# Kernel optimization log

Measured on AMD Instinct MI355X. Metric: run time of the kernel, lower is better.

## Reference

```python
import jax, jax.numpy as jnp
import numpy as np

L, D = 2048, 1024
D_INNER = 2 * D          # expand=2
D_STATE = 16
D_CONV = 4
DT_RANK = D // 16        # ceil(1024/16) = 64
HID = 4 * D
EPS = 1e-5


def _layernorm(x, g, b):
    mu = jnp.mean(x, axis=-1, keepdims=True)
    var = jnp.mean(jnp.square(x - mu), axis=-1, keepdims=True)
    return (x - mu) * jax.lax.rsqrt(var + EPS) * g + b


def setup_inputs() -> dict:
    key = jax.random.key(0)
    ks = jax.random.split(key, 12)
    f = lambda k, sh, s=0.02: (jax.random.normal(k, sh, jnp.float32) * s)
    return {
        "x": jax.random.normal(ks[0], (L, D), jnp.float32),
        "ln1_g": jnp.ones((D,), jnp.float32),
        "ln1_b": jnp.zeros((D,), jnp.float32),
        "ln2_g": jnp.ones((D,), jnp.float32),
        "ln2_b": jnp.zeros((D,), jnp.float32),
        "in_proj_w": f(ks[1], (2 * D_INNER, D)),
        "conv_w": f(ks[2], (D_INNER, D_CONV), 0.1),
        "conv_b": jnp.zeros((D_INNER,), jnp.float32),
        "x_proj_w": f(ks[3], (DT_RANK + 2 * D_STATE, D_INNER)),
        "dt_proj_w": f(ks[4], (D_INNER, DT_RANK), 0.1),
        "dt_proj_b": f(ks[5], (D_INNER,), 0.1),
        "A_log": jnp.log(jnp.broadcast_to(
            jnp.arange(1, D_STATE + 1, dtype=jnp.float32), (D_INNER, D_STATE))),
        "D_param": jnp.ones((D_INNER,), jnp.float32),
        "out_proj_w": f(ks[6], (D, D_INNER)),
        "ffn_w1": f(ks[7], (HID, D)),
        "ffn_b1": jnp.zeros((HID,), jnp.float32),
        "ffn_w2": f(ks[8], (D, HID)),
        "ffn_b2": jnp.zeros((D,), jnp.float32),
    }


def _mamba(x, in_proj_w, conv_w, conv_b, x_proj_w, dt_proj_w, dt_proj_b,
           A_log, D_param, out_proj_w):
    # x: (L, D)
    xz = x @ in_proj_w.T                    # (L, 2*d_inner)
    xm, z = xz[:, :D_INNER], xz[:, D_INNER:]
    # causal depthwise conv1d, kernel d_conv, output length L
    xp = jnp.pad(xm, ((D_CONV - 1, 0), (0, 0)))
    xc = conv_b
    for k in range(D_CONV):                 # 4 taps, fixed small loop
        xc = xc + xp[k:k + L] * conv_w[None, :, k]
    xc = jax.nn.silu(xc)                    # (L, d_inner)
    proj = xc @ x_proj_w.T                  # (L, dt_rank + 2*d_state)
    dt = proj[:, :DT_RANK]
    B = proj[:, DT_RANK:DT_RANK + D_STATE]  # (L, d_state)
    C = proj[:, DT_RANK + D_STATE:]         # (L, d_state)
    delta = jax.nn.softplus(dt @ dt_proj_w.T + dt_proj_b)  # (L, d_inner)
    A = -jnp.exp(A_log)                     # (d_inner, d_state)
    dA = jnp.exp(delta[:, :, None] * A[None])               # (L, d_inner, d_state)
    dBx = delta[:, :, None] * B[:, None, :] * xc[:, :, None]

    def step(h, inp):
        dA_t, dBx_t, C_t = inp
        h = h * dA_t + dBx_t                # (d_inner, d_state)
        y = jnp.einsum('ds,s->d', h, C_t)
        return h, y

    h0 = jnp.zeros((D_INNER, D_STATE), x.dtype)
    _, ys = jax.lax.scan(step, h0, (dA, dBx, C))            # ys: (L, d_inner)
    y = ys + xc * D_param
    y = y * jax.nn.silu(z)
    return y @ out_proj_w.T                 # (L, D)


def reference(x, ln1_g, ln1_b, ln2_g, ln2_b, in_proj_w, conv_w, conv_b,
              x_proj_w, dt_proj_w, dt_proj_b, A_log, D_param, out_proj_w,
              ffn_w1, ffn_b1, ffn_w2, ffn_b2):
    residual = x
    h = _layernorm(x, ln1_g, ln1_b)
    h = _mamba(h, in_proj_w, conv_w, conv_b, x_proj_w, dt_proj_w, dt_proj_b,
               A_log, D_param, out_proj_w)
    h = h + residual
    # FFN has an internal residual around the normed input, plus outer residual
    n = _layernorm(h, ln2_g, ln2_b)
    f = n + (jax.nn.relu(n @ ffn_w1.T + ffn_b1) @ ffn_w2.T + ffn_b2)
    return h + f
```

## Files before the change

### kernel.cpp

```cpp
#include <hip/hip_runtime.h>
#include <hip/hip_bf16.h>
#include <math.h>

#define L_SEQ 2048
#define DMODEL 1024
#define DINNER 2048
#define DSTATE 16
#define DTRANK 64
#define NHID 4096
#define NC 64
#define LC 32

typedef __bf16 bf16_t;
typedef __bf16 bf16x4 __attribute__((ext_vector_type(4)));
typedef __bf16 bf16x8 __attribute__((ext_vector_type(8)));
typedef float f32x4 __attribute__((ext_vector_type(4)));

#define WAIT_VM0 0x0F70

__device__ __forceinline__ void async_cp16(const bf16_t* g, bf16_t* l) {
    __builtin_amdgcn_global_load_lds(
        (const __attribute__((address_space(1))) void*)g,
        (__attribute__((address_space(3))) void*)l, 16, 0, 0);
}

template <int EPI, int SPLIT>
__global__ __launch_bounds__(512, 4) void gemm_big(
    const bf16_t* __restrict__ A, int lda,
    const bf16_t* __restrict__ W, int ldw,
    bf16_t* __restrict__ C, int ldc,
    int Kslice, long cstride,
    const float* __restrict__ bias)
{
    __shared__ bf16_t As[2 * 8192];
    __shared__ bf16_t Ws[2 * 4096];

    const int tid  = threadIdx.x;
    const int lane = tid & 63;
    const int w    = tid >> 6;

    int my, mx, kz;
    if (SPLIT == 0) {
        int lid = blockIdx.y * 32 + blockIdx.x;
        int r = lid & 7, i = lid >> 3;
        my = (r >> 2) * 4 + (i & 3);
        mx = (r & 3) * 8 + (i >> 2);
        kz = 0;
    } else {
        int id = (blockIdx.z * 8 + blockIdx.y) * 8 + blockIdx.x;
        int r = id & 7, i = id >> 3;
        kz = r >> 1;
        my = i & 7;
        mx = (r & 1) * 4 + (i >> 3);
    }
    const int m0 = my * 256;
    const int n0 = mx * 128;
    const int k0 = kz * Kslice;

    const int p    = lane & 3;
    const int rA0  = 2 * w * 16 + (lane >> 2);
    const int rA1  = rA0 + 16;
    const int rW   = w * 16 + (lane >> 2);
    const int dcA0 = (p - ((rA0 >> 1) & 3)) & 3;
    const int dcA1 = (p - ((rA1 >> 1) & 3)) & 3;
    const int dcW  = (p - ((rW  >> 1) & 3)) & 3;

    const bf16_t* gA0 = A + (size_t)(m0 + rA0) * lda + k0 + dcA0 * 8;
    const bf16_t* gA1 = A + (size_t)(m0 + rA1) * lda + k0 + dcA1 * 8;
    const bf16_t* gW  = W + (size_t)(n0 + rW) * ldw + k0 + dcW * 8;
    const int aLo0 = (2 * w) * 512;
    const int aLo1 = aLo0 + 512;
    const int wLo  = w * 512;

    const int wr   = w >> 1;
    const int wc   = w & 1;
    const int quad = lane >> 4;
    const int lr   = lane & 15;
    int offA[4], offW[4];
    #pragma unroll
    for (int i = 0; i < 4; ++i) {
        int ra = wr * 64 + i * 16 + lr;
        offA[i] = ra * 32 + (((quad + ((ra >> 1) & 3)) & 3) * 8);
        int rb = wc * 64 + i * 16 + lr;
        offW[i] = rb * 32 + (((quad + ((rb >> 1) & 3)) & 3) * 8);
    }

    const int niter = Kslice >> 5;

    async_cp16(gA0, &As[aLo0]);
    async_cp16(gA1, &As[aLo1]);
    async_cp16(gW,  &Ws[wLo]);
    gA0 += 32; gA1 += 32; gW += 32;

    f32x4 acc[4][4] = {};
    for (int it = 0; it < niter; ++it) {
        __builtin_amdgcn_s_waitcnt(WAIT_VM0);
        __builtin_amdgcn_s_barrier();
        asm volatile("" ::: "memory");

        if (it + 1 < niter) {
            int sa = ((it + 1) & 1) * 8192;
            int sw = ((it + 1) & 1) * 4096;
            async_cp16(gA0, &As[sa + aLo0]);
            async_cp16(gA1, &As[sa + aLo1]);
            async_cp16(gW,  &Ws[sw + wLo]);
            gA0 += 32; gA1 += 32; gW += 32;
        }

        const int ca = (it & 1) * 8192;
        const int cw = (it & 1) * 4096;
        bf16x8 af[4], bw[4];
        #pragma unroll
        for (int i = 0; i < 4; ++i) af[i] = *(const bf16x8*)&As[ca + offA[i]];
        #pragma unroll
        for (int j = 0; j < 4; ++j) bw[j] = *(const bf16x8*)&Ws[cw + offW[j]];
        #pragma unroll
        for (int i = 0; i < 4; ++i)
            #pragma unroll
            for (int j = 0; j < 4; ++j)
                acc[i][j] = __builtin_amdgcn_mfma_f32_16x16x32_bf16(af[i], bw[j], acc[i][j], 0, 0, 0);
    }

    bf16_t* Cb = C + (size_t)kz * cstride;
    #pragma unroll
    for (int i = 0; i < 4; ++i) {
        int row0 = m0 + wr * 64 + i * 16 + quad * 4;
        #pragma unroll
        for (int j = 0; j < 4; ++j) {
            int col = n0 + wc * 64 + j * 16 + lr;
            float bv = (EPI == 2) ? bias[col] : 0.f;
            #pragma unroll
            for (int r = 0; r < 4; ++r) {
                float v = acc[i][j][r];
                if (EPI == 2) v = fmaxf(v + bv, 0.f);
                Cb[(size_t)(row0 + r) * ldc + col] = (bf16_t)v;
            }
        }
    }
}

template <int EPI, int OUTBF16>
__global__ __launch_bounds__(256) void gemm_simple(
    const bf16_t* __restrict__ A, int lda,
    const bf16_t* __restrict__ W, int ldw,
    void* __restrict__ Cv, int ldc,
    int N, int Kslice, long cstride,
    const float* __restrict__ bias)
{
    __shared__ bf16_t As[128 * 72];
    __shared__ bf16_t Ws[128 * 72];

    const int tid  = threadIdx.x;
    const int lane = tid & 63;
    const int w    = tid >> 6;
    const int m0   = blockIdx.y * 128;
    const int n0   = blockIdx.x * 128;
    const int kz   = blockIdx.z;
    const int k0   = kz * Kslice;

    const int wr   = w >> 1;
    const int wc   = w & 1;
    const int quad = lane >> 4;
    const int lr   = lane & 15;

    f32x4 acc[4][4] = {};

    for (int k = 0; k < Kslice; k += 64) {
        __syncthreads();
        #pragma unroll
        for (int i = 0; i < 4; ++i) {
            int idx = tid + i * 256;
            int row = idx >> 3;
            int c8  = (idx & 7) * 8;
            *(bf16x8*)&As[row * 72 + c8] =
                *(const bf16x8*)(A + (size_t)(m0 + row) * lda + k0 + k + c8);
            int gn = n0 + row; if (gn > N - 1) gn = N - 1;
            *(bf16x8*)&Ws[row * 72 + c8] =
                *(const bf16x8*)(W + (size_t)gn * ldw + k0 + k + c8);
        }
        __syncthreads();

        #pragma unroll
        for (int kk = 0; kk < 64; kk += 32) {
            bf16x8 af[4], bw[4];
            #pragma unroll
            for (int i = 0; i < 4; ++i)
                af[i] = *(const bf16x8*)&As[(wr * 64 + i * 16 + lr) * 72 + kk + quad * 8];
            #pragma unroll
            for (int j = 0; j < 4; ++j)
                bw[j] = *(const bf16x8*)&Ws[(wc * 64 + j * 16 + lr) * 72 + kk + quad * 8];
            #pragma unroll
            for (int i = 0; i < 4; ++i)
                #pragma unroll
                for (int j = 0; j < 4; ++j)
                    acc[i][j] = __builtin_amdgcn_mfma_f32_16x16x32_bf16(af[i], bw[j], acc[i][j], 0, 0, 0);
        }
    }

    float*  Cf = (float*)Cv + (size_t)kz * cstride;
    bf16_t* Cb = (bf16_t*)Cv + (size_t)kz * cstride;
    #pragma unroll
    for (int i = 0; i < 4; ++i) {
        int row0 = m0 + wr * 64 + i * 16 + quad * 4;
        #pragma unroll
        for (int j = 0; j < 4; ++j) {
            int col = n0 + wc * 64 + j * 16 + lr;
            if (col < N) {
                float bv = (EPI == 3) ? bias[col] : 0.f;
                #pragma unroll
                for (int r = 0; r < 4; ++r) {
                    float v = acc[i][j][r];
                    if (EPI == 3) {
                        float t = v + bv;
                        v = fmaxf(t, 0.f) + log1pf(__expf(-fabsf(t)));
                    }
                    size_t o = (size_t)(row0 + r) * ldc + col;
                    if (OUTBF16) Cb[o] = (bf16_t)v;
                    else         Cf[o] = v;
                }
            }
        }
    }
}

__global__ __launch_bounds__(256) void cvt_ln1(
    const float* __restrict__ s0, const float* __restrict__ s1,
    const float* __restrict__ s2, const float* __restrict__ s3,
    const float* __restrict__ s4, const float* __restrict__ s5,
    bf16_t* __restrict__ dst,
    const float* __restrict__ x, const float* __restrict__ g,
    const float* __restrict__ b, bf16_t* __restrict__ outb)
{
    if (blockIdx.x < 14656) {
        int e = (blockIdx.x * 256 + threadIdx.x) * 4;
        const float* src; int local;
        if      (e < 4194304)  { src = s0; local = e; }
        else if (e < 4390912)  { src = s1; local = e - 4194304; }
        else if (e < 4521984)  { src = s2; local = e - 4390912; }
        else if (e < 6619136)  { src = s3; local = e - 4521984; }
        else if (e < 10813440) { src = s4; local = e - 6619136; }
        else                   { src = s5; local = e - 10813440; }
        float4 v = *(const float4*)(src + local);
        bf16x4 o;
        o[0] = (bf16_t)v.x; o[1] = (bf16_t)v.y; o[2] = (bf16_t)v.z; o[3] = (bf16_t)v.w;
        *(bf16x4*)(dst + e) = o;
        return;
    }
    const int row = blockIdx.x - 14656;
    const float* xr = x + (size_t)row * DMODEL;
    float v[4];
    float s = 0.f, sq = 0.f;
    #pragma unroll
    for (int i = 0; i < 4; ++i) {
        v[i] = xr[threadIdx.x + i * 256];
        s += v[i]; sq += v[i] * v[i];
    }
    #pragma unroll
    for (int off = 32; off > 0; off >>= 1) {
        s += __shfl_xor(s, off); sq += __shfl_xor(sq, off);
    }
    __shared__ float rs_[4], rq_[4];
    int w = threadIdx.x >> 6;
    if ((threadIdx.x & 63) == 0) { rs_[w] = s; rq_[w] = sq; }
    __syncthreads();
    s  = rs_[0] + rs_[1] + rs_[2] + rs_[3];
    sq = rq_[0] + rq_[1] + rq_[2] + rq_[3];
    float mu  = s * (1.f / DMODEL);
    float var = sq * (1.f / DMODEL) - mu * mu;
    float rsd = rsqrtf(var + 1e-5f);
    #pragma unroll
    for (int i = 0; i < 4; ++i) {
        int col = threadIdx.x + i * 256;
        outb[(size_t)row * DMODEL + col] = (bf16_t)((v[i] - mu) * rsd * g[col] + b[col]);
    }
}

__global__ __launch_bounds__(256) void conv_silu(
    const bf16_t* __restrict__ xz, const float* __restrict__ cw,
    const float* __restrict__ cb, bf16_t* __restrict__ xc)
{
    int gid = blockIdx.x * 256 + threadIdx.x;
    int c = gid & (DINNER - 1);
    int t = gid >> 11;
    float acc = cb[c];
    #pragma unroll
    for (int k = 0; k < 4; ++k) {
        int tt = t + k - 3;
        if (tt >= 0) acc += (float)xz[(size_t)tt * (2 * DINNER) + c] * cw[c * 4 + k];
    }
    float sig = 1.f / (1.f + __expf(-acc));
    xc[gid] = (bf16_t)(acc * sig);
}

__global__ __launch_bounds__(256) void scan_pass1(
    const bf16_t* __restrict__ delta, const bf16_t* __restrict__ xc,
    const float* __restrict__ proj, const float* __restrict__ A_log,
    float* __restrict__ carryH, float* __restrict__ sumd)
{
    const int c = blockIdx.x;
    const int d = blockIdx.y * 256 + threadIdx.x;
    const int t0 = c * LC;

    __shared__ float Bs[LC][DSTATE];
    for (int i = threadIdx.x; i < LC * DSTATE; i += 256) {
        int tt = i >> 4, s = i & 15;
        Bs[tt][s] = proj[(size_t)(t0 + tt) * 96 + DTRANK + s];
    }
    __syncthreads();

    float a[DSTATE], h[DSTATE];
    #pragma unroll
    for (int s = 0; s < DSTATE; ++s) {
        a[s] = -__expf(A_log[d * DSTATE + s]);
        h[s] = 0.f;
    }
    float sd = 0.f;
    float dl = (float)delta[(size_t)t0 * DINNER + d];
    float x  = (float)xc[(size_t)t0 * DINNER + d];
    for (int i = 0; i < LC; ++i) {
        float dln = 0.f, xn = 0.f;
        if (i + 1 < LC) {
            dln = (float)delta[(size_t)(t0 + i + 1) * DINNER + d];
            xn  = (float)xc[(size_t)(t0 + i + 1) * DINNER + d];
        }
        sd += dl;
        float dx = dl * x;
        #pragma unroll
        for (int s = 0; s < DSTATE; ++s)
            h[s] = h[s] * __expf(dl * a[s]) + dx * Bs[i][s];
        dl = dln; x = xn;
    }
    #pragma unroll
    for (int s = 0; s < DSTATE; ++s)
        carryH[((size_t)c * DINNER + d) * DSTATE + s] = h[s];
    sumd[c * DINNER + d] = sd;
}

__global__ __launch_bounds__(256) void scan_pass2(
    const float* __restrict__ A_log, const float* __restrict__ carryH,
    const float* __restrict__ sumd, float* __restrict__ hinit)
{
    int idx = blockIdx.x * 256 + threadIdx.x;
    int d = idx >> 4;
    float a = -__expf(A_log[idx]);
    float hc = 0.f;
    for (int c0 = 0; c0 < NC; c0 += 8) {
        float H[8], P[8];
        #pragma unroll
        for (int j = 0; j < 8; ++j) {
            H[j] = carryH[(size_t)(c0 + j) * (DINNER * DSTATE) + idx];
            P[j] = __expf(a * sumd[(c0 + j) * DINNER + d]);
        }
        #pragma unroll
        for (int j = 0; j < 8; ++j) {
            hinit[(size_t)(c0 + j) * (DINNER * DSTATE) + idx] = hc;
            hc = H[j] + P[j] * hc;
        }
    }
}

__global__ __launch_bounds__(256) void scan_pass3(
    const bf16_t* __restrict__ delta, const bf16_t* __restrict__ xc,
    const float* __restrict__ proj, const float* __restrict__ A_log,
    const float* __restrict__ hinit, const float* __restrict__ Dp,
    const bf16_t* __restrict__ xz, bf16_t* __restrict__ yact)
{
    const int c = blockIdx.x;
    const int d = blockIdx.y * 256 + threadIdx.x;
    const int t0 = c * LC;

    __shared__ float Bs[LC][DSTATE], Cs[LC][DSTATE];
    for (int i = threadIdx.x; i < LC * DSTATE; i += 256) {
        int tt = i >> 4, s = i & 15;
        size_t base = (size_t)(t0 + tt) * 96;
        Bs[tt][s] = proj[base + DTRANK + s];
        Cs[tt][s] = proj[base + DTRANK + DSTATE + s];
    }
    __syncthreads();

    float a[DSTATE], h[DSTATE];
    #pragma unroll
    for (int s = 0; s < DSTATE; ++s) {
        a[s] = -__expf(A_log[d * DSTATE + s]);
        h[s] = hinit[(size_t)c * (DINNER * DSTATE) + d * DSTATE + s];
    }
    float DD = Dp[d];
    float dl = (float)delta[(size_t)t0 * DINNER + d];
    float x  = (float)xc[(size_t)t0 * DINNER + d];
    float z  = (float)xz[(size_t)t0 * (2 * DINNER) + DINNER + d];
    for (int i = 0; i < LC; ++i) {
        float dln = 0.f, xn = 0.f, zn = 0.f;
        if (i + 1 < LC) {
            int tn = t0 + i + 1;
            dln = (float)delta[(size_t)tn * DINNER + d];
            xn  = (float)xc[(size_t)tn * DINNER + d];
            zn  = (float)xz[(size_t)tn * (2 * DINNER) + DINNER + d];
        }
        float dx = dl * x;
        float y = 0.f;
        #pragma unroll
        for (int s = 0; s < DSTATE; ++s) {
            h[s] = h[s] * __expf(dl * a[s]) + dx * Bs[i][s];
            y += h[s] * Cs[i][s];
        }
        float yv = y + x * DD;
        float sil = z / (1.f + __expf(-z));
        yact[(size_t)(t0 + i) * DINNER + d] = (bf16_t)(yv * sil);
        dl = dln; x = xn; z = zn;
    }
}

__global__ __launch_bounds__(256) void reduce4(
    const float* __restrict__ part, float* __restrict__ proj,
    bf16_t* __restrict__ projdt)
{
    int i = blockIdx.x * 256 + threadIdx.x;
    float v = 0.f;
    #pragma unroll
    for (int s = 0; s < 16; ++s) v += part[(size_t)s * 196608 + i];
    proj[i] = v;
    int row = i / 96;
    int col = i - row * 96;
    if (col < DTRANK) projdt[row * DTRANK + col] = (bf16_t)v;
}

__global__ __launch_bounds__(256) void red9_ln2(
    const bf16_t* __restrict__ part, const float* __restrict__ x,
    const float* __restrict__ g, const float* __restrict__ b,
    float* __restrict__ hres, float* __restrict__ nbuf,
    bf16_t* __restrict__ nbufb)
{
    const int row = blockIdx.x;
    const size_t base = (size_t)row * DMODEL;
    float v[4];
    float s = 0.f, sq = 0.f;
    #pragma unroll
    for (int i = 0; i < 4; ++i) {
        int col = threadIdx.x + i * 256;
        float acc = x[base + col];
        #pragma unroll
        for (int sl = 0; sl < 4; ++sl)
            acc += (float)part[(size_t)sl * 2097152 + base + col];
        hres[base + col] = acc;
        v[i] = acc; s += acc; sq += acc * acc;
    }
    #pragma unroll
    for (int off = 32; off > 0; off >>= 1) {
        s += __shfl_xor(s, off); sq += __shfl_xor(sq, off);
    }
    __shared__ float rs_[4], rq_[4];
    int w = threadIdx.x >> 6;
    if ((threadIdx.x & 63) == 0) { rs_[w] = s; rq_[w] = sq; }
    __syncthreads();
    s  = rs_[0] + rs_[1] + rs_[2] + rs_[3];
    sq = rq_[0] + rq_[1] + rq_[2] + rq_[3];
    float mu  = s * (1.f / DMODEL);
    float var = sq * (1.f / DMODEL) - mu * mu;
    float rsd = rsqrtf(var + 1e-5f);
    #pragma unroll
    for (int i = 0; i < 4; ++i) {
        int col = threadIdx.x + i * 256;
        float o = (v[i] - mu) * rsd * g[col] + b[col];
        nbuf[base + col] = o;
        nbufb[base + col] = (bf16_t)o;
    }
}

__global__ __launch_bounds__(256) void reduce12(
    const bf16_t* __restrict__ part, const float* __restrict__ b2,
    const float* __restrict__ hres, const float* __restrict__ nbuf,
    float* __restrict__ out)
{
    int i = (blockIdx.x * 256 + threadIdx.x) * 4;
    float4 bb = *(const float4*)(b2 + (i & (DMODEL - 1)));
    float4 h  = *(const float4*)(hres + i);
    float4 n  = *(const float4*)(nbuf + i);
    float s0 = bb.x + h.x + n.x, s1 = bb.y + h.y + n.y;
    float s2 = bb.z + h.z + n.z, s3 = bb.w + h.w + n.w;
    #pragma unroll
    for (int sl = 0; sl < 4; ++sl) {
        bf16x4 v = *(const bf16x4*)(part + (size_t)sl * 2097152 + i);
        s0 += (float)v[0]; s1 += (float)v[1]; s2 += (float)v[2]; s3 += (float)v[3];
    }
    *(float4*)(out + i) = make_float4(s0, s1, s2, s3);
}

extern "C" void kernel_launch(void* const* d_in, const int* in_sizes, int n_in,
                              void* d_out, int out_size, void* d_ws, size_t ws_size,
                              hipStream_t stream)
{
    const float* x        = (const float*)d_in[0];
    const float* ln1_g    = (const float*)d_in[1];
    const float* ln1_b    = (const float*)d_in[2];
    const float* ln2_g    = (const float*)d_in[3];
    const float* ln2_b    = (const float*)d_in[4];
    const float* in_proj  = (const float*)d_in[5];
    const float* conv_w   = (const float*)d_in[6];
    const float* conv_b   = (const float*)d_in[7];
    const float* x_proj   = (const float*)d_in[8];
    const float* dt_proj  = (const float*)d_in[9];
    const float* dt_b     = (const float*)d_in[10];
    const float* A_log    = (const float*)d_in[11];
    const float* D_param  = (const float*)d_in[12];
    const float* out_proj = (const float*)d_in[13];
    const float* ffn_w1   = (const float*)d_in[14];
    const float* ffn_b1   = (const float*)d_in[15];
    const float* ffn_w2   = (const float*)d_in[16];
    const float* ffn_b2   = (const float*)d_in[17];
    float* out = (float*)d_out;

    char* base = (char*)d_ws;
    bf16_t* Wb     = (bf16_t*)(base);
    bf16_t* w_inp  = Wb;
    bf16_t* w_xp   = Wb + 4194304;
    bf16_t* w_dtp  = Wb + 4390912;
    bf16_t* w_outp = Wb + 4521984;
    bf16_t* w_f1   = Wb + 6619136;
    bf16_t* w_f2   = Wb + 10813440;

    bf16_t* h1b    = (bf16_t*)(base + 30015488);
    float*  proj   = (float*)(base + 30015488);
    bf16_t* projdt = (bf16_t*)(base + 30015488 + 786432);
    bf16_t* xz     = (bf16_t*)(base + 34209792);
    bf16_t* ffnh   = xz;
    bf16_t* xc     = (bf16_t*)(base + 50987008);
    float*  part   = (float*)(base + 59375616);
    bf16_t* delta  = (bf16_t*)part;
    bf16_t* partb  = (bf16_t*)part;
    float*  carry  = (float*)(base + 76152832);
    bf16_t* nbufb  = (bf16_t*)carry;
    float*  sumd   = (float*)(base + 84541440);
    float*  hinit  = (float*)(base + 85065728);
    float*  nbuf   = hinit;
    bf16_t* yact   = (bf16_t*)(base + 93454336);
    float*  hres   = (float*)(base + 101842944);

    cvt_ln1<<<14656 + 2048, 256, 0, stream>>>(in_proj, x_proj, dt_proj, out_proj,
                                              ffn_w1, ffn_w2, Wb,
                                              x, ln1_g, ln1_b, h1b);
    gemm_big<0, 0><<<dim3(32, 8), 512, 0, stream>>>(
        h1b, DMODEL, w_inp, DMODEL, xz, 4096, 1024, 0, nullptr);
    conv_silu<<<(L_SEQ * DINNER) / 256, 256, 0, stream>>>(xz, conv_w, conv_b, xc);
    gemm_simple<0, 0><<<dim3(1, 16, 16), 256, 0, stream>>>(
        xc, DINNER, w_xp, DINNER, part, 96, 96, 128, 196608L, nullptr);
    reduce4<<<768, 256, 0, stream>>>(part, proj, projdt);
    gemm_simple<3, 1><<<dim3(16, 16, 1), 256, 0, stream>>>(
        projdt, DTRANK, w_dtp, DTRANK, delta, DINNER, DINNER, DTRANK, 0, dt_b);
    scan_pass1<<<dim3(NC, DINNER / 256), 256, 0, stream>>>(delta, xc, proj, A_log, carry, sumd);
    scan_pass2<<<(DINNER * DSTATE) / 256, 256, 0, stream>>>(A_log, carry, sumd, hinit);
    scan_pass3<<<dim3(NC, DINNER / 256), 256, 0, stream>>>(delta, xc, proj, A_log, hinit,
                                                           D_param, xz, yact);
    gemm_big<0, 1><<<dim3(8, 8, 4), 512, 0, stream>>>(
        yact, DINNER, w_outp, DINNER, partb, DMODEL, 512, 2097152L, nullptr);
    red9_ln2<<<L_SEQ, 256, 0, stream>>>(partb, x, ln2_g, ln2_b, hres, nbuf, nbufb);
    gemm_big<2, 0><<<dim3(32, 8), 512, 0, stream>>>(
        nbufb, DMODEL, w_f1, DMODEL, ffnh, NHID, 1024, 0, ffn_b1);
    gemm_big<0, 1><<<dim3(8, 8, 4), 512, 0, stream>>>(
        ffnh, NHID, w_f2, NHID, partb, DMODEL, 1024, 2097152L, nullptr);
    reduce12<<<2048, 256, 0, stream>>>(partb, ffn_b2, hres, nbuf, out);
}
```

Before: 403.0 us.

## Fuse dt_proj GEMM and softplus into scan passes; drop x_proj split-K

Removes the separate dt_proj GEMM and the delta buffer. Each scan chunk block now computes its 32x256 delta tile with MFMA from the projected dt rows and the dt_proj weights, applies bias and softplus, and keeps the result in LDS. The x_proj GEMM no longer uses split-K with a reduce kernel and instead writes proj directly over the full K=2048 loop, which saves two launches but leaves only 16 blocks for that GEMM. The delta tile is computed twice, once in pass 1 and once in pass 3, and the scan loops lose their manual next-step prefetch.

```diff
diff --git a/kernel.cpp b/kernel.cpp
--- a/kernel.cpp
+++ b/kernel.cpp
@@ -206,14 +206,9 @@
         for (int j = 0; j < 4; ++j) {
             int col = n0 + wc * 64 + j * 16 + lr;
             if (col < N) {
-                float bv = (EPI == 3) ? bias[col] : 0.f;
                 #pragma unroll
                 for (int r = 0; r < 4; ++r) {
                     float v = acc[i][j][r];
-                    if (EPI == 3) {
-                        float t = v + bv;
-                        v = fmaxf(t, 0.f) + log1pf(__expf(-fabsf(t)));
-                    }
                     size_t o = (size_t)(row0 + r) * ldc + col;
                     if (OUTBF16) Cb[o] = (bf16_t)v;
                     else         Cf[o] = v;
@@ -292,19 +287,63 @@
     xc[gid] = (bf16_t)(acc * sig);
 }
 
-__global__ __launch_bounds__(256) void scan_pass1(
-    const bf16_t* __restrict__ delta, const bf16_t* __restrict__ xc,
-    const float* __restrict__ proj, const float* __restrict__ A_log,
+__global__ __launch_bounds__(256) void scan1f(
+    const float* __restrict__ proj, const bf16_t* __restrict__ wdt,
+    const float* __restrict__ dtb, const bf16_t* __restrict__ xc,
+    const float* __restrict__ A_log,
     float* __restrict__ carryH, float* __restrict__ sumd)
 {
-    const int c = blockIdx.x;
-    const int d = blockIdx.y * 256 + threadIdx.x;
-    const int t0 = c * LC;
-
-    __shared__ float Bs[LC][DSTATE];
-    for (int i = threadIdx.x; i < LC * DSTATE; i += 256) {
+    const int c   = blockIdx.x;
+    const int g   = blockIdx.y;
+    const int tid = threadIdx.x;
+    const int t0  = c * LC;
+    const int d   = g * 256 + tid;
+
+    __shared__ bf16_t dtA[32 * 72];
+    __shared__ bf16_t Wd[256 * 72];
+    __shared__ float  deltaS[32 * 257];
+    __shared__ float  Bs[LC][DSTATE];
+
+    for (int idx = tid; idx < 32 * 64; idx += 256) {
+        int t = idx >> 6, k = idx & 63;
+        dtA[t * 72 + k] = (bf16_t)proj[(size_t)(t0 + t) * 96 + k];
+    }
+    for (int idx = tid; idx < 256 * 8; idx += 256) {
+        int n = idx >> 3, ch = idx & 7;
+        *(bf16x8*)&Wd[n * 72 + ch * 8] =
+            *(const bf16x8*)(wdt + (size_t)(g * 256 + n) * 64 + ch * 8);
+    }
+    for (int i = tid; i < LC * DSTATE; i += 256) {
         int tt = i >> 4, s = i & 15;
         Bs[tt][s] = proj[(size_t)(t0 + tt) * 96 + DTRANK + s];
+    }
+    __syncthreads();
+
+    {
+        const int w = tid >> 6, lane = tid & 63;
+        const int quad = lane >> 4, lr = lane & 15;
+        const int cb = w * 64;
+        #pragma unroll
+        for (int jt = 0; jt < 4; ++jt) {
+            #pragma unroll
+            for (int mt = 0; mt < 2; ++mt) {
+                f32x4 acc = {};
+                bf16x8 a0 = *(const bf16x8*)&dtA[(mt * 16 + lr) * 72 + quad * 8];
+                bf16x8 a1 = *(const bf16x8*)&dtA[(mt * 16 + lr) * 72 + 32 + quad * 8];
+                bf16x8 b0 = *(const bf16x8*)&Wd[(cb + jt * 16 + lr) * 72 + quad * 8];
+                bf16x8 b1 = *(const bf16x8*)&Wd[(cb + jt * 16 + lr) * 72 + 32 + quad * 8];
+                acc = __builtin_amdgcn_mfma_f32_16x16x32_bf16(a0, b0, acc, 0, 0, 0);
+                acc = __builtin_amdgcn_mfma_f32_16x16x32_bf16(a1, b1, acc, 0, 0, 0);
+                int col = cb + jt * 16 + lr;
+                float bv = dtb[g * 256 + col];
+                #pragma unroll
+                for (int r = 0; r < 4; ++r) {
+                    int row = mt * 16 + quad * 4 + r;
+                    float t = acc[r] + bv;
+                    deltaS[row * 257 + col] = fmaxf(t, 0.f) + log1pf(__expf(-fabsf(t)));
+                }
+            }
+        }
     }
     __syncthreads();
 
@@ -315,20 +354,14 @@
         h[s] = 0.f;
     }
     float sd = 0.f;
-    float dl = (float)delta[(size_t)t0 * DINNER + d];
-    float x  = (float)xc[(size_t)t0 * DINNER + d];
     for (int i = 0; i < LC; ++i) {
-        float dln = 0.f, xn = 0.f;
-        if (i + 1 < LC) {
-            dln = (float)delta[(size_t)(t0 + i + 1) * DINNER + d];
-            xn  = (float)xc[(size_t)(t0 + i + 1) * DINNER + d];
-        }
+        float dl = deltaS[i * 257 + tid];
+        float x  = (float)xc[(size_t)(t0 + i) * DINNER + d];
         sd += dl;
         float dx = dl * x;
         #pragma unroll
         for (int s = 0; s < DSTATE; ++s)
             h[s] = h[s] * __expf(dl * a[s]) + dx * Bs[i][s];
-        dl = dln; x = xn;
     }
     #pragma unroll
     for (int s = 0; s < DSTATE; ++s)
@@ -359,18 +392,34 @@
     }
 }
 
-__global__ __launch_bounds__(256) void scan_pass3(
-    const bf16_t* __restrict__ delta, const bf16_t* __restrict__ xc,
-    const float* __restrict__ proj, const float* __restrict__ A_log,
-    const float* __restrict__ hinit, const float* __restrict__ Dp,
-    const bf16_t* __restrict__ xz, bf16_t* __restrict__ yact)
-{
-    const int c = blockIdx.x;
-    const int d = blockIdx.y * 256 + threadIdx.x;
-    const int t0 = c * LC;
-
-    __shared__ float Bs[LC][DSTATE], Cs[LC][DSTATE];
-    for (int i = threadIdx.x; i < LC * DSTATE; i += 256) {
+__global__ __launch_bounds__(256) void scan3f(
+    const float* __restrict__ proj, const bf16_t* __restrict__ wdt,
+    const float* __restrict__ dtb, const bf16_t* __restrict__ xc,
+    const float* __restrict__ A_log, const float* __restrict__ hinit,
+    const float* __restrict__ Dp, const bf16_t* __restrict__ xz,
+    bf16_t* __restrict__ yact)
+{
+    const int c   = blockIdx.x;
+    const int g   = blockIdx.y;
+    const int tid = threadIdx.x;
+    const int t0  = c * LC;
+    const int d   = g * 256 + tid;
+
+    __shared__ bf16_t dtA[32 * 72];
+    __shared__ bf16_t Wd[256 * 72];
+    __shared__ float  deltaS[32 * 257];
+    __shared__ float  Bs[LC][DSTATE], Cs[LC][DSTATE];
+
+    for (int idx = tid; idx < 32 * 64; idx += 256) {
+        int t = idx >> 6, k = idx & 63;
+        dtA[t * 72 + k] = (bf16_t)proj[(size_t)(t0 + t) * 96 + k];
+    }
+    for (int idx = tid; idx < 256 * 8; idx += 256) {
+        int n = idx >> 3, ch = idx & 7;
+        *(bf16x8*)&Wd[n * 72 + ch * 8] =
+            *(const bf16x8*)(wdt + (size_t)(g * 256 + n) * 64 + ch * 8);
+    }
+    for (int i = tid; i < LC * DSTATE; i += 256) {
         int tt = i >> 4, s = i & 15;
         size_t base = (size_t)(t0 + tt) * 96;
         Bs[tt][s] = proj[base + DTRANK + s];
@@ -378,6 +427,34 @@
     }
     __syncthreads();
 
+    {
+        const int w = tid >> 6, lane = tid & 63;
+        const int quad = lane >> 4, lr = lane & 15;
+        const int cb = w * 64;
+        #pragma unroll
+        for (int jt = 0; jt < 4; ++jt) {
+            #pragma unroll
+            for (int mt = 0; mt < 2; ++mt) {
+                f32x4 acc = {};
+                bf16x8 a0 = *(const bf16x8*)&dtA[(mt * 16 + lr) * 72 + quad * 8];
+                bf16x8 a1 = *(const bf16x8*)&dtA[(mt * 16 + lr) * 72 + 32 + quad * 8];
+                bf16x8 b0 = *(const bf16x8*)&Wd[(cb + jt * 16 + lr) * 72 + quad * 8];
+                bf16x8 b1 = *(const bf16x8*)&Wd[(cb + jt * 16 + lr) * 72 + 32 + quad * 8];
+                acc = __builtin_amdgcn_mfma_f32_16x16x32_bf16(a0, b0, acc, 0, 0, 0);
+                acc = __builtin_amdgcn_mfma_f32_16x16x32_bf16(a1, b1, acc, 0, 0, 0);
+                int col = cb + jt * 16 + lr;
+                float bv = dtb[g * 256 + col];
+                #pragma unroll
+                for (int r = 0; r < 4; ++r) {
+                    int row = mt * 16 + quad * 4 + r;
+                    float t = acc[r] + bv;
+                    deltaS[row * 257 + col] = fmaxf(t, 0.f) + log1pf(__expf(-fabsf(t)));
+                }
+            }
+        }
+    }
+    __syncthreads();
+
     float a[DSTATE], h[DSTATE];
     #pragma unroll
     for (int s = 0; s < DSTATE; ++s) {
@@ -385,17 +462,10 @@
         h[s] = hinit[(size_t)c * (DINNER * DSTATE) + d * DSTATE + s];
     }
     float DD = Dp[d];
-    float dl = (float)delta[(size_t)t0 * DINNER + d];
-    float x  = (float)xc[(size_t)t0 * DINNER + d];
-    float z  = (float)xz[(size_t)t0 * (2 * DINNER) + DINNER + d];
     for (int i = 0; i < LC; ++i) {
-        float dln = 0.f, xn = 0.f, zn = 0.f;
-        if (i + 1 < LC) {
-            int tn = t0 + i + 1;
-            dln = (float)delta[(size_t)tn * DINNER + d];
-            xn  = (float)xc[(size_t)tn * DINNER + d];
-            zn  = (float)xz[(size_t)tn * (2 * DINNER) + DINNER + d];
-        }
+        int t = t0 + i;
+        float dl = deltaS[i * 257 + tid];
+        float x  = (float)xc[(size_t)t * DINNER + d];
         float dx = dl * x;
         float y = 0.f;
         #pragma unroll
@@ -404,24 +474,10 @@
             y += h[s] * Cs[i][s];
         }
         float yv = y + x * DD;
+        float z = (float)xz[(size_t)t * (2 * DINNER) + DINNER + d];
         float sil = z / (1.f + __expf(-z));
-        yact[(size_t)(t0 + i) * DINNER + d] = (bf16_t)(yv * sil);
-        dl = dln; x = xn; z = zn;
-    }
-}
-
-__global__ __launch_bounds__(256) void reduce4(
-    const float* __restrict__ part, float* __restrict__ proj,
-    bf16_t* __restrict__ projdt)
-{
-    int i = blockIdx.x * 256 + threadIdx.x;
-    float v = 0.f;
-    #pragma unroll
-    for (int s = 0; s < 16; ++s) v += part[(size_t)s * 196608 + i];
-    proj[i] = v;
-    int row = i / 96;
-    int col = i - row * 96;
-    if (col < DTRANK) projdt[row * DTRANK + col] = (bf16_t)v;
+        yact[(size_t)t * DINNER + d] = (bf16_t)(yv * sil);
+    }
 }
 
 __global__ __launch_bounds__(256) void red9_ln2(
@@ -519,19 +575,16 @@
     bf16_t* w_f2   = Wb + 10813440;
 
     bf16_t* h1b    = (bf16_t*)(base + 30015488);
-    float*  proj   = (float*)(base + 30015488);
-    bf16_t* projdt = (bf16_t*)(base + 30015488 + 786432);
+    float*  proj   = (float*)(base + 31064064);
     bf16_t* xz     = (bf16_t*)(base + 34209792);
     bf16_t* ffnh   = xz;
     bf16_t* xc     = (bf16_t*)(base + 50987008);
-    float*  part   = (float*)(base + 59375616);
-    bf16_t* delta  = (bf16_t*)part;
-    bf16_t* partb  = (bf16_t*)part;
+    bf16_t* partb  = (bf16_t*)(base + 59375616);
     float*  carry  = (float*)(base + 76152832);
-    bf16_t* nbufb  = (bf16_t*)carry;
     float*  sumd   = (float*)(base + 84541440);
     float*  hinit  = (float*)(base + 85065728);
     float*  nbuf   = hinit;
+    bf16_t* nbufb  = (bf16_t*)carry;
     bf16_t* yact   = (bf16_t*)(base + 93454336);
     float*  hres   = (float*)(base + 101842944);
 
@@ -541,15 +594,12 @@
     gemm_big<0, 0><<<dim3(32, 8), 512, 0, stream>>>(
         h1b, DMODEL, w_inp, DMODEL, xz, 4096, 1024, 0, nullptr);
     conv_silu<<<(L_SEQ * DINNER) / 256, 256, 0, stream>>>(xz, conv_w, conv_b, xc);
-    gemm_simple<0, 0><<<dim3(1, 16, 16), 256, 0, stream>>>(
-        xc, DINNER, w_xp, DINNER, part, 96, 96, 128, 196608L, nullptr);
-    reduce4<<<768, 256, 0, stream>>>(part, proj, projdt);
-    gemm_simple<3, 1><<<dim3(16, 16, 1), 256, 0, stream>>>(
-        projdt, DTRANK, w_dtp, DTRANK, delta, DINNER, DINNER, DTRANK, 0, dt_b);
-    scan_pass1<<<dim3(NC, DINNER / 256), 256, 0, stream>>>(delta, xc, proj, A_log, carry, sumd);
+    gemm_simple<0, 0><<<dim3(1, 16, 1), 256, 0, stream>>>(
+        xc, DINNER, w_xp, DINNER, proj, 96, 96, 2048, 0, nullptr);
+    scan1f<<<dim3(NC, 8), 256, 0, stream>>>(proj, w_dtp, dt_b, xc, A_log, carry, sumd);
     scan_pass2<<<(DINNER * DSTATE) / 256, 256, 0, stream>>>(A_log, carry, sumd, hinit);
-    scan_pass3<<<dim3(NC, DINNER / 256), 256, 0, stream>>>(delta, xc, proj, A_log, hinit,
-                                                           D_param, xz, yact);
+    scan3f<<<dim3(NC, 8), 256, 0, stream>>>(proj, w_dtp, dt_b, xc, A_log, hinit,
+                                            D_param, xz, yact);
     gemm_big<0, 1><<<dim3(8, 8, 4), 512, 0, stream>>>(
         yact, DINNER, w_outp, DINNER, partb, DMODEL, 512, 2097152L, nullptr);
     red9_ln2<<<L_SEQ, 256, 0, stream>>>(partb, x, ln2_g, ln2_b, hres, nbuf, nbufb);
```

New measurement: 395.9 us. About the same (-1.8%).
